# Performance work log

Hardware: AMD Instinct MI355X
Metric: run time of the kernel (lower is better)

Reference implementation:

```python
import jax, jax.numpy as jnp
import numpy as np

K = 30          # hard-coded in Hypergraph.from_feature_kNN(ft, k=30)
BN_EPS = 1e-5   # BatchNorm1d eval mode, running_mean=0, running_var=1


def setup_inputs() -> dict:
    key = jax.random.key(0)
    ks = jax.random.split(key, 3)
    B, C, H, W = 8, 64, 56, 56
    hid = 32
    return {
        "x": jax.random.normal(ks[0], (B, C, H, W), jnp.float32),
        "w1": jax.random.normal(ks[1], (C, hid), jnp.float32) / np.sqrt(C).astype(np.float32),
        "b1": jnp.zeros((hid,), jnp.float32),
        "g1": jnp.ones((hid,), jnp.float32),
        "be1": jnp.zeros((hid,), jnp.float32),
        "w2": jax.random.normal(ks[2], (hid, C), jnp.float32) / np.sqrt(hid).astype(np.float32),
        "b2": jnp.zeros((C,), jnp.float32),
        "g2": jnp.ones((C,), jnp.float32),
        "be2": jnp.zeros((C,), jnp.float32),
    }


def _knn_idx(ft, k):
    # squared euclidean distances via gram trick; same ordering as torch.cdist
    sq = jnp.sum(ft * ft, axis=1)
    d2 = sq[:, None] + sq[None, :] - 2.0 * (ft @ ft.T)   # [L, L]
    _, idx = jax.lax.top_k(-d2, k)                        # k smallest distances (incl. self)
    return idx                                            # [L, k] -> hyperedge e = kNN of vertex e


def _v2v_mean(X, nbr):
    # hg.v2v(X, aggr="mean"): v2e mean then e2v mean over the kNN incidence structure
    L, k = nbr.shape
    F = X.shape[1]
    Y = jnp.mean(X[nbr], axis=1)                                        # v2e: [L_edges, F]
    seg = nbr.reshape(-1)                                               # vertex nbr[e,j] belongs to edge e
    vals = jnp.broadcast_to(Y[:, None, :], (L, k, F)).reshape(L * k, F)
    s = jax.ops.segment_sum(vals, seg, num_segments=L)                  # e2v sum
    dv = jax.ops.segment_sum(jnp.ones((L * k,), X.dtype), seg, num_segments=L)
    return s / jnp.maximum(dv, 1.0)[:, None]                            # e2v mean


def _bn_eval(x, g, b):
    # BatchNorm1d in eval: running_mean=0, running_var=1
    return x * (g * np.float32(1.0 / np.sqrt(1.0 + BN_EPS))) + b


def reference(x, w1, b1, g1, be1, w2, b2, g2, be2):
    B, C, H, W = x.shape
    L = H * W
    xf = x.reshape(B, L, C)  # faithful raw x.view(B, L, C) (no transpose in source)

    def per_sample(ft):
        nbr = _knn_idx(ft, K)
        # HGNNPConv 1: theta -> bn -> v2v(mean) -> relu (dropout off in eval)
        h = _bn_eval(ft @ w1 + b1, g1, be1)
        h = jax.nn.relu(_v2v_mean(h, nbr))
        # HGNNPConv 2 (is_last): theta -> bn -> v2v(mean), no act/drop
        h = _bn_eval(h @ w2 + b2, g2, be2)
        return _v2v_mean(h, nbr)  # [L, C]

    outs = jax.vmap(per_sample)(xf)      # [B, L, C]
    return outs.reshape(B, -1, H, W)     # faithful raw outs.view(B, -1, H, W)
```

## Files before the change

kernel.cpp:

```cpp
#include <hip/hip_runtime.h>
#include <math.h>


namespace {

constexpr int cB = 8;
constexpr int cL = 3136;
constexpr int cC = 64;
constexpr int cH = 32;
constexpr int cK = 30;
constexpr int NV = cB * cL;
constexpr int QD = 10;
constexpr float BN_SC = 0.99999500003749964f;

typedef __bf16 bf16x4 __attribute__((ext_vector_type(4)));
typedef __bf16 bf16x8 __attribute__((ext_vector_type(8)));
typedef float floatx4 __attribute__((ext_vector_type(4)));

__device__ inline unsigned umin2(unsigned a, unsigned b) { return a < b ? a : b; }
__device__ inline unsigned umax2(unsigned a, unsigned b) { return a > b ? a : b; }
__device__ inline unsigned umin3(unsigned a, unsigned b, unsigned c) {
  return umin2(umin2(a, b), c);
}
__device__ inline float bf16lo(unsigned u) { return __uint_as_float(u << 16); }
__device__ inline float bf16hi(unsigned u) {
  return __uint_as_float(u & 0xFFFF0000u);
}

__device__ inline unsigned bclean64(unsigned v, int ln) {
#pragma unroll
  for (int off = 32; off; off >>= 1) {
    unsigned p = (unsigned)__shfl_xor((int)v, off);
    v = (ln & off) ? umax2(v, p) : umin2(v, p);
  }
  return v;
}

__global__ void k_split(const float* __restrict__ x, ushort* __restrict__ xhi,
                        ushort* __restrict__ xlo, float* __restrict__ sqf,
                        int* __restrict__ cnt, int* __restrict__ cur) {
  int v = blockIdx.x * 256 + threadIdx.x;
  if (v >= NV) return;
  cnt[v] = 0;
  cur[v] = 0;
  const float4* p = reinterpret_cast<const float4*>(x) + (size_t)v * 16;
  double s = 0.0;
#pragma unroll
  for (int c = 0; c < 16; ++c) {
    float4 f = p[c];
    bf16x4 hh, ll;
#pragma unroll
    for (int e = 0; e < 4; ++e) {
      float a = (&f.x)[e];
      __bf16 h = (__bf16)a;
      ll[e] = (__bf16)(a - (float)h);
      hh[e] = h;
      s += (double)a * (double)a;
    }
    *reinterpret_cast<bf16x4*>(&xhi[(size_t)v * 64 + c * 4]) = hh;
    *reinterpret_cast<bf16x4*>(&xlo[(size_t)v * 64 + c * 4]) = ll;
  }
  sqf[v] = (float)(s * 64.0 + 32768.0);
}

__global__ __launch_bounds__(128, 4) void k_sweep(
    const ushort* __restrict__ xhi, const ushort* __restrict__ xlo,
    const float* __restrict__ sqf, unsigned* __restrict__ candq) {
  const int ib = blockIdx.x, qt = blockIdx.y, b = blockIdx.z;
  const int r0 = ib * 32;
  const int jb0 = qt * 768;
  const int ntile = (qt == 3) ? 26 : 24;
  const size_t bbase = (size_t)b * cL;

  __shared__ ushort aHi[32 * 72], aLo[32 * 72];
  __shared__ ushort bHi[32 * 72], bLo[32 * 72];
  __shared__ float sqJs[32];

  const int t  = threadIdx.x;
  const int ln = t & 63;
  const int w  = t >> 6;
  const int tx = ln & 15;
  const int qd = ln >> 4;

#pragma unroll
  for (int it = 0; it < 2; ++it) {
    int idx = t + 128 * it;
    int r = idx >> 3, blk = idx & 7;
    *reinterpret_cast<uint4*>(&aHi[r * 72 + blk * 8]) =
        *reinterpret_cast<const uint4*>(&xhi[(bbase + r0 + r) * 64 + blk * 8]);
    *reinterpret_cast<uint4*>(&aLo[r * 72 + blk * 8]) =
        *reinterpret_cast<const uint4*>(&xlo[(bbase + r0 + r) * 64 + blk * 8]);
  }
  __syncthreads();

  bf16x8 aH[2], aL[2];
#pragma unroll
  for (int kk = 0; kk < 2; ++kk) {
    aH[kk] = *reinterpret_cast<const bf16x8*>(
        &aHi[(w * 16 + tx) * 72 + kk * 32 + qd * 8]);
    aL[kk] = *reinterpret_cast<const bf16x8*>(
        &aLo[(w * 16 + tx) * 72 + kk * 32 + qd * 8]);
  }

  unsigned q[4][QD];
#pragma unroll
  for (int e = 0; e < 4; ++e)
#pragma unroll
    for (int k = 0; k < QD; ++k) q[e][k] = 0xFFFFFFFFu;

  for (int st = 0; st < ntile; ++st) {
    const int jb = jb0 + st * 32;
#pragma unroll
    for (int it = 0; it < 2; ++it) {
      int idx = t + 128 * it;
      int r = idx >> 3, blk = idx & 7;
      *reinterpret_cast<uint4*>(&bHi[r * 72 + blk * 8]) =
          *reinterpret_cast<const uint4*>(&xhi[(bbase + jb + r) * 64 + blk * 8]);
      *reinterpret_cast<uint4*>(&bLo[r * 72 + blk * 8]) =
          *reinterpret_cast<const uint4*>(&xlo[(bbase + jb + r) * 64 + blk * 8]);
    }
    if (t < 32) sqJs[t] = sqf[bbase + jb + t];
    __syncthreads();

    unsigned pk[2][4];
#pragma unroll
    for (int f = 0; f < 2; ++f) {
      const int bro = (f * 16 + tx) * 72 + qd * 8;
      bf16x8 bh0 = *reinterpret_cast<const bf16x8*>(&bHi[bro]);
      bf16x8 bh1 = *reinterpret_cast<const bf16x8*>(&bHi[bro + 32]);
      bf16x8 bl0 = *reinterpret_cast<const bf16x8*>(&bLo[bro]);
      bf16x8 bl1 = *reinterpret_cast<const bf16x8*>(&bLo[bro + 32]);
      floatx4 acc = {0.f, 0.f, 0.f, 0.f};
      acc = __builtin_amdgcn_mfma_f32_16x16x32_bf16(aH[0], bh0, acc, 0, 0, 0);
      acc = __builtin_amdgcn_mfma_f32_16x16x32_bf16(aH[1], bh1, acc, 0, 0, 0);
      acc = __builtin_amdgcn_mfma_f32_16x16x32_bf16(aH[0], bl0, acc, 0, 0, 0);
      acc = __builtin_amdgcn_mfma_f32_16x16x32_bf16(aH[1], bl1, acc, 0, 0, 0);
      acc = __builtin_amdgcn_mfma_f32_16x16x32_bf16(aL[0], bh0, acc, 0, 0, 0);
      acc = __builtin_amdgcn_mfma_f32_16x16x32_bf16(aL[1], bh1, acc, 0, 0, 0);
      const float sjs = sqJs[f * 16 + tx];
      const unsigned col = (unsigned)(jb + f * 16 + tx);
#pragma unroll
      for (int e = 0; e < 4; ++e) {
        float qf = fmaf(acc[e], -128.f, sjs);
        qf = fminf(fmaxf(qf, 0.f), 65535.f);
        pk[f][e] = ((unsigned)qf << 12) | col;
      }
    }

#pragma unroll
    for (int e = 0; e < 4; ++e) {
      unsigned a0 = umin2(pk[0][e], pk[1][e]);
      unsigned a1 = umax2(pk[0][e], pk[1][e]);
#pragma unroll
      for (int i = QD - 1; i >= 2; --i)
        q[e][i] = umin3(q[e][i], umax2(q[e][i - 1], a0),
                        umax2(q[e][i - 2], a1));
      q[e][1] = umin3(q[e][1], umax2(q[e][0], a0), a1);
      q[e][0] = umin3(q[e][0], a0, a1);
    }
    __syncthreads();
  }

  unsigned* cr[4];
#pragma unroll
  for (int e = 0; e < 4; ++e)
    cr[e] = candq + (bbase + r0 + w * 16 + qd * 4 + e) * 160 + qt * 40;
  for (int it = 0; it < 40; ++it) {
    unsigned h0 = q[0][0], h1 = q[1][0], h2 = q[2][0], h3 = q[3][0];
    unsigned m0 = h0, m1 = h1, m2 = h2, m3 = h3;
#pragma unroll
    for (int off = 1; off < 16; off <<= 1) {
      m0 = umin2(m0, (unsigned)__shfl_xor((int)m0, off));
      m1 = umin2(m1, (unsigned)__shfl_xor((int)m1, off));
      m2 = umin2(m2, (unsigned)__shfl_xor((int)m2, off));
      m3 = umin2(m3, (unsigned)__shfl_xor((int)m3, off));
    }
    if (tx == 0) {
      cr[0][it] = m0;
      cr[1][it] = m1;
      cr[2][it] = m2;
      cr[3][it] = m3;
    }
    if (h0 == m0) {
#pragma unroll
      for (int k = 0; k < QD - 1; ++k) q[0][k] = q[0][k + 1];
      q[0][QD - 1] = 0xFFFFFFFFu;
    }
    if (h1 == m1) {
#pragma unroll
      for (int k = 0; k < QD - 1; ++k) q[1][k] = q[1][k + 1];
      q[1][QD - 1] = 0xFFFFFFFFu;
    }
    if (h2 == m2) {
#pragma unroll
      for (int k = 0; k < QD - 1; ++k) q[2][k] = q[2][k + 1];
      q[2][QD - 1] = 0xFFFFFFFFu;
    }
    if (h3 == m3) {
#pragma unroll
      for (int k = 0; k < QD - 1; ++k) q[3][k] = q[3][k + 1];
      q[3][QD - 1] = 0xFFFFFFFFu;
    }
  }
}

__global__ __launch_bounds__(256) void k_rescore(const float* __restrict__ x,
                                                 const unsigned* __restrict__ candq,
                                                 int* __restrict__ nbr,
                                                 int* __restrict__ cnt) {
  const int w  = threadIdx.x >> 6;
  const int ln = threadIdx.x & 63;
  const size_t row = (size_t)blockIdx.x * 4 + w;
  const size_t bvert = row - (row % cL);

  const unsigned* cq = candq + row * 160;
  unsigned A = (ln < 40) ? cq[ln]       : 0xFFFFFFFFu;
  unsigned B = (ln < 40) ? cq[40 + ln]  : 0xFFFFFFFFu;
  unsigned C = (ln < 40) ? cq[80 + ln]  : 0xFFFFFFFFu;
  unsigned D = (ln < 40) ? cq[120 + ln] : 0xFFFFFFFFu;

  unsigned s1 = umin2(A, (unsigned)__shfl((int)B, 63 - ln));
  s1 = bclean64(s1, ln);
  unsigned s2 = umin2(C, (unsigned)__shfl((int)D, 63 - ln));
  s2 = bclean64(s2, ln);
  unsigned g = umin2(s1, (unsigned)__shfl((int)s2, 63 - ln));
  g = bclean64(g, ln);

  const unsigned qv = g >> 12;
  const int col = min((int)(g & 0xFFFu), cL - 1);

  unsigned q29 = (unsigned)__shfl((int)qv, 29);
  unsigned q30 = (unsigned)__shfl((int)qv, 30);
  if (q30 > q29 + 3) {
    if (ln < cK) {
      nbr[row * cK + ln] = col;
      atomicAdd(&cnt[bvert + col], 1);
    }
    return;
  }

  float4 xi[16];
  const float4* xi4 = reinterpret_cast<const float4*>(x + row * 64);
#pragma unroll
  for (int c = 0; c < 16; ++c) xi[c] = xi4[c];

  double dv = 1e300;
  if (ln < 40) {
    const float4* xj4 = reinterpret_cast<const float4*>(x + (bvert + col) * 64);
    double ax = 0.0, ay = 0.0, az = 0.0, aw = 0.0;
#pragma unroll
    for (int c = 0; c < 16; ++c) {
      float4 xj = xj4[c];
      double d0 = (double)xi[c].x - (double)xj.x; ax = fma(d0, d0, ax);
      double d1 = (double)xi[c].y - (double)xj.y; ay = fma(d1, d1, ay);
      double d2 = (double)xi[c].z - (double)xj.z; az = fma(d2, d2, az);
      double d3 = (double)xi[c].w - (double)xj.w; aw = fma(d3, d3, aw);
    }
    dv = (ax + ay) + (az + aw);
  }
  int r2 = 0;
  for (int j = 0; j < 40; ++j) {
    double od = __shfl(dv, j);
    r2 += (od < dv || (od == dv && j < ln)) ? 1 : 0;
  }
  if (ln < 40 && r2 < cK) {
    nbr[row * cK + r2] = col;
    atomicAdd(&cnt[bvert + col], 1);
  }
}

__global__ void k_scan(const int* __restrict__ cnt, int* __restrict__ rp) {
  int b = blockIdx.x;
  int ln = threadIdx.x;
  const int* c = cnt + b * cL;
  int* r = rp + b * (cL + 1);
  int carry = 0;
  for (int base = 0; base < cL; base += 64) {
    int v = c[base + ln];
    int s = v;
#pragma unroll
    for (int off = 1; off < 64; off <<= 1) {
      int u = __shfl_up(s, off);
      if (ln >= off) s += u;
    }
    r[base + ln] = carry + s - v;
    carry += __shfl(s, 63);
  }
  if (ln == 63) r[cL] = carry;
}

__global__ void k_fill(const int* __restrict__ nbr, const int* __restrict__ rp,
                       int* __restrict__ cur, int* __restrict__ el) {
  int g = blockIdx.x * 256 + threadIdx.x;
  if (g >= NV * cK) return;
  int b = g / (cL * cK);
  int e = (g / cK) % cL;
  int v = nbr[g];
  v = min(max(v, 0), cL - 1);
  int p = rp[b * (cL + 1) + v] + atomicAdd(&cur[b * cL + v], 1);
  p = min(max(p, 0), cL * cK - 1);
  el[(size_t)b * cL * cK + p] = e;
}

__global__ __launch_bounds__(256) void k_theta1(const float* __restrict__ x,
                                                const float* __restrict__ w1,
                                                const float* __restrict__ b1,
                                                const float* __restrict__ g1,
                                                const float* __restrict__ be1,
                                                __bf16* __restrict__ h1) {
  __shared__ float w[cC * cH];
  int t = threadIdx.x;
  for (int n = t; n < cC * cH; n += 256) w[n] = w1[n];
  __syncthreads();
  int g = blockIdx.x * 256 + t;
  int row = g >> 5;
  int f = g & 31;
  const float4* xr = reinterpret_cast<const float4*>(x) + (size_t)row * 16;
  float s = 0.f;
#pragma unroll
  for (int kc = 0; kc < 16; ++kc) {
    float4 xv = xr[kc];
    s += xv.x * w[(4 * kc + 0) * cH + f];
    s += xv.y * w[(4 * kc + 1) * cH + f];
    s += xv.z * w[(4 * kc + 2) * cH + f];
    s += xv.w * w[(4 * kc + 3) * cH + f];
  }
  h1[g] = (__bf16)((s + b1[f]) * (g1[f] * BN_SC) + be1[f]);
}

__global__ __launch_bounds__(256) void k_v2e32(const __bf16* __restrict__ X,
                                               const int* __restrict__ nbr,
                                               __bf16* __restrict__ Y) {
  const int w  = threadIdx.x >> 6;
  const int ln = threadIdx.x & 63;
  const size_t er = (size_t)blockIdx.x * 4 + w;
  const size_t b  = er / cL;
  const __bf16* Xb = X + b * cL * cH;
  const int nb_l = nbr[er * cK + (ln < cK ? ln : cK - 1)];
  const int hi = ln >> 5, f = ln & 31;
  int idx[15];
#pragma unroll
  for (int m = 0; m < 15; ++m) idx[m] = __shfl(nb_l, hi + 2 * m);
  float y[15];
#pragma unroll
  for (int m = 0; m < 15; ++m) y[m] = (float)Xb[(size_t)idx[m] * cH + f];
  float s = 0.f;
#pragma unroll
  for (int m = 0; m < 15; ++m) s += y[m];
  s += __shfl_xor(s, 32);
  if (hi == 0) Y[er * cH + f] = (__bf16)(s * (1.f / 30.f));
}

__global__ __launch_bounds__(256) void k_e2v_t2(const __bf16* __restrict__ Y,
                                                const int* __restrict__ rp,
                                                const int* __restrict__ el,
                                                const float* __restrict__ w2,
                                                const float* __restrict__ b2,
                                                const float* __restrict__ g2,
                                                const float* __restrict__ be2,
                                                __bf16* __restrict__ h2) {
  __shared__ float w2s[cH * cC];
  {
    int t = threadIdx.x;
    for (int n = t; n < cH * cC; n += 256) w2s[n] = w2[n];
  }
  const int w  = threadIdx.x >> 6;
  const int ln = threadIdx.x & 63;
  const size_t vr = (size_t)blockIdx.x * 4 + w;
  const size_t b  = vr / cL;
  const int v = (int)(vr % cL);
  const int* rpb = rp + b * (cL + 1);
  const int s0 = rpb[v];
  const int deg = rpb[v + 1] - s0;
  const int* elb = el + b * (size_t)cL * cK + s0;
  const __bf16* Yb = Y + b * cL * cH;
  const int hi = ln >> 5, f = ln & 31;
  float s = 0.f;

  for (int base = 0; base < deg; base += 64) {
    const int take = min(64, deg - base);
    const int eidx = elb[base + (ln < take ? ln : 0)];
    for (int j0 = 0; j0 < take; j0 += 16) {
      float acc = 0.f;
#pragma unroll
      for (int k2 = 0; k2 < 8; ++k2) {
        int j = j0 + 2 * k2 + hi;
        int e0 = __shfl(eidx, j < take ? j : 0);
        float y = (float)Yb[(size_t)e0 * cH + f];
        acc += (j < take) ? y : 0.f;
      }
      s += acc;
    }
  }
  __syncthreads();

  s += __shfl_xor(s, 32);
  float r = fmaxf(s / (float)deg, 0.f);

  float s2 = 0.f;
#pragma unroll 8
  for (int k = 0; k < cH; ++k) {
    float rk = __shfl(r, k);
    s2 = fmaf(rk, w2s[k * cC + ln], s2);
  }
  h2[vr * cC + ln] = (__bf16)((s2 + b2[ln]) * (g2[ln] * BN_SC) + be2[ln]);
}

__global__ __launch_bounds__(256) void k_v2e64(const __bf16* __restrict__ X,
                                               const int* __restrict__ nbr,
                                               __bf16* __restrict__ Y) {
  const int w  = threadIdx.x >> 6;
  const int ln = threadIdx.x & 63;
  const size_t er = (size_t)blockIdx.x * 4 + w;
  const size_t b  = er / cL;
  const unsigned* Xb = reinterpret_cast<const unsigned*>(X + b * cL * cC);
  const int nb_l = nbr[er * cK + (ln < cK ? ln : cK - 1)];
  const int half = ln >> 5, f2 = ln & 31;
  int idx[15];
#pragma unroll
  for (int m = 0; m < 15; ++m) idx[m] = __shfl(nb_l, 2 * m + half);
  unsigned v[15];
#pragma unroll
  for (int m = 0; m < 15; ++m) v[m] = Xb[(size_t)idx[m] * 32 + f2];
  float s0 = 0.f, s1 = 0.f;
#pragma unroll
  for (int m = 0; m < 15; ++m) {
    s0 += bf16lo(v[m]);
    s1 += bf16hi(v[m]);
  }
  s0 += __shfl_xor(s0, 32);
  s1 += __shfl_xor(s1, 32);
  if (half == 0) {
    union {
      __bf16 h[2];
      unsigned u;
    } cv;
    cv.h[0] = (__bf16)(s0 * (1.f / 30.f));
    cv.h[1] = (__bf16)(s1 * (1.f / 30.f));
    reinterpret_cast<unsigned*>(Y)[er * 32 + f2] = cv.u;
  }
}

__global__ __launch_bounds__(256) void k_e2v64(const __bf16* __restrict__ Y,
                                               const int* __restrict__ rp,
                                               const int* __restrict__ el,
                                               float* __restrict__ out) {
  const int w  = threadIdx.x >> 6;
  const int ln = threadIdx.x & 63;
  const size_t vr = (size_t)blockIdx.x * 4 + w;
  const size_t b  = vr / cL;
  const int v = (int)(vr % cL);
  const int* rpb = rp + b * (cL + 1);
  const int s0r = rpb[v];
  const int deg = rpb[v + 1] - s0r;
  const int* elb = el + b * (size_t)cL * cK + s0r;
  const unsigned* Yb = reinterpret_cast<const unsigned*>(Y + b * cL * cC);
  const int half = ln >> 5, f2 = ln & 31;
  float s0 = 0.f, s1 = 0.f;

  for (int base = 0; base < deg; base += 64) {
    const int take = min(64, deg - base);
    const int eidx = elb[base + (ln < take ? ln : 0)];
    for (int j0 = 0; j0 < take; j0 += 16) {
      float a0 = 0.f, a1 = 0.f;
#pragma unroll
      for (int k2 = 0; k2 < 8; ++k2) {
        int j = j0 + 2 * k2 + half;
        int e0 = __shfl(eidx, j < take ? j : 0);
        unsigned u = Yb[(size_t)e0 * 32 + f2];
        bool ok = j < take;
        a0 += ok ? bf16lo(u) : 0.f;
        a1 += ok ? bf16hi(u) : 0.f;
      }
      s0 += a0;
      s1 += a1;
    }
  }
  s0 += __shfl_xor(s0, 32);
  s1 += __shfl_xor(s1, 32);
  float v0 = __shfl(s0, ln >> 1);
  float v1 = __shfl(s1, ln >> 1);
  out[vr * cC + ln] = ((ln & 1) ? v1 : v0) / (float)deg;
}

}

extern "C" void kernel_launch(void* const* d_in, const int* in_sizes, int n_in,
                              void* d_out, int out_size, void* d_ws,
                              size_t ws_size, hipStream_t stream) {
  (void)in_sizes; (void)n_in; (void)out_size; (void)ws_size;
  const float* x   = (const float*)d_in[0];
  const float* w1  = (const float*)d_in[1];
  const float* b1  = (const float*)d_in[2];
  const float* g1  = (const float*)d_in[3];
  const float* be1 = (const float*)d_in[4];
  const float* w2  = (const float*)d_in[5];
  const float* b2  = (const float*)d_in[6];
  const float* g2  = (const float*)d_in[7];
  const float* be2 = (const float*)d_in[8];
  float* out = (float*)d_out;

  char* base = (char*)d_ws;
  size_t off = 0;
  auto carve = [&](size_t bytes) {
    char* p = base + off;
    off += (bytes + 255) & ~(size_t)255;
    return p;
  };
  float* sqf = (float*)carve((size_t)NV * 4);
  int*   nbr = (int*)carve((size_t)NV * cK * 4);
  int*   rp  = (int*)carve((size_t)cB * (cL + 1) * 4);
  int*   cnt = (int*)carve((size_t)NV * 4);
  int*   cur = (int*)carve((size_t)NV * 4);
  char* RA = carve((size_t)NV * 64 * 2 * 2);
  ushort* xhi = (ushort*)RA;
  ushort* xlo = (ushort*)(RA + 3211264);
  int* el = (int*)RA;
  char* RC = carve((size_t)NV * 160 * 4);
  unsigned* candq = (unsigned*)RC;
  __bf16* h1 = (__bf16*)RC;
  __bf16* Y1 = (__bf16*)(RC + 1605632);
  __bf16* h2 = (__bf16*)(RC + 3211264);
  __bf16* Y2 = (__bf16*)(RC + 6422528);

  k_split<<<(NV + 255) / 256, 256, 0, stream>>>(x, xhi, xlo, sqf, cnt, cur);
  k_sweep<<<dim3(98, 4, cB), 128, 0, stream>>>(xhi, xlo, sqf, candq);
  k_rescore<<<NV / 4, 256, 0, stream>>>(x, candq, nbr, cnt);

  k_scan<<<cB, 64, 0, stream>>>(cnt, rp);
  k_fill<<<(NV * cK) / 256, 256, 0, stream>>>(nbr, rp, cur, el);

  k_theta1<<<NV * cH / 256, 256, 0, stream>>>(x, w1, b1, g1, be1, h1);
  k_v2e32<<<NV / 4, 256, 0, stream>>>(h1, nbr, Y1);
  k_e2v_t2<<<NV / 4, 256, 0, stream>>>(Y1, rp, el, w2, b2, g2, be2, h2);
  k_v2e64<<<NV / 4, 256, 0, stream>>>(h2, nbr, Y2);
  k_e2v64<<<NV / 4, 256, 0, stream>>>(Y2, rp, el, out);
}
```

Before: 425.1 us.

## Prefetch next B tile into registers in kNN sweep and parallelize scan

The kNN sweep kernel now loads the next 32-column tile of hi/lo bf16 features and squared norms into registers while the MFMA and top-k queue work runs on the current tile. The loads are written to shared memory at the top of the next iteration, so global latency overlaps with compute. A sched_barrier keeps the compiler from moving the prefetch. The per-batch prefix scan moves from one 64-thread wave looping serially over 3136 entries to a 1024-thread block doing a wave scan plus a cross-wave sum. In exchange the sweep uses more registers and the scan uses shared memory and a block barrier.

```diff
diff --git a/kernel.cpp b/kernel.cpp
--- a/kernel.cpp
+++ b/kernel.cpp
@@ -108,19 +108,37 @@
 #pragma unroll
     for (int k = 0; k < QD; ++k) q[e][k] = 0xFFFFFFFFu;
 
+  const int pr  = (t + 0)   >> 3, pblk  = (t + 0)   & 7;
+  const int pr1 = (t + 128) >> 3, pblk1 = (t + 128) & 7;
+  uint4 pH0, pH1, pL0, pL1;
+  float pS = 0.f;
+  {
+    const int jb = jb0;
+    pH0 = *reinterpret_cast<const uint4*>(&xhi[(bbase + jb + pr) * 64 + pblk * 8]);
+    pL0 = *reinterpret_cast<const uint4*>(&xlo[(bbase + jb + pr) * 64 + pblk * 8]);
+    pH1 = *reinterpret_cast<const uint4*>(&xhi[(bbase + jb + pr1) * 64 + pblk1 * 8]);
+    pL1 = *reinterpret_cast<const uint4*>(&xlo[(bbase + jb + pr1) * 64 + pblk1 * 8]);
+    if (t < 32) pS = sqf[bbase + jb + t];
+  }
+
   for (int st = 0; st < ntile; ++st) {
-    const int jb = jb0 + st * 32;
-#pragma unroll
-    for (int it = 0; it < 2; ++it) {
-      int idx = t + 128 * it;
-      int r = idx >> 3, blk = idx & 7;
-      *reinterpret_cast<uint4*>(&bHi[r * 72 + blk * 8]) =
-          *reinterpret_cast<const uint4*>(&xhi[(bbase + jb + r) * 64 + blk * 8]);
-      *reinterpret_cast<uint4*>(&bLo[r * 72 + blk * 8]) =
-          *reinterpret_cast<const uint4*>(&xlo[(bbase + jb + r) * 64 + blk * 8]);
-    }
-    if (t < 32) sqJs[t] = sqf[bbase + jb + t];
     __syncthreads();
+    *reinterpret_cast<uint4*>(&bHi[pr * 72 + pblk * 8])   = pH0;
+    *reinterpret_cast<uint4*>(&bLo[pr * 72 + pblk * 8])   = pL0;
+    *reinterpret_cast<uint4*>(&bHi[pr1 * 72 + pblk1 * 8]) = pH1;
+    *reinterpret_cast<uint4*>(&bLo[pr1 * 72 + pblk1 * 8]) = pL1;
+    if (t < 32) sqJs[t] = pS;
+    __syncthreads();
+
+    if (st + 1 < ntile) {
+      const int jb = jb0 + (st + 1) * 32;
+      pH0 = *reinterpret_cast<const uint4*>(&xhi[(bbase + jb + pr) * 64 + pblk * 8]);
+      pL0 = *reinterpret_cast<const uint4*>(&xlo[(bbase + jb + pr) * 64 + pblk * 8]);
+      pH1 = *reinterpret_cast<const uint4*>(&xhi[(bbase + jb + pr1) * 64 + pblk1 * 8]);
+      pL1 = *reinterpret_cast<const uint4*>(&xlo[(bbase + jb + pr1) * 64 + pblk1 * 8]);
+      if (t < 32) pS = sqf[bbase + jb + t];
+    }
+    __builtin_amdgcn_sched_barrier(0);
 
     unsigned pk[2][4];
 #pragma unroll
@@ -138,7 +156,7 @@
       acc = __builtin_amdgcn_mfma_f32_16x16x32_bf16(aL[0], bh0, acc, 0, 0, 0);
       acc = __builtin_amdgcn_mfma_f32_16x16x32_bf16(aL[1], bh1, acc, 0, 0, 0);
       const float sjs = sqJs[f * 16 + tx];
-      const unsigned col = (unsigned)(jb + f * 16 + tx);
+      const unsigned col = (unsigned)(jb0 + st * 32 + f * 16 + tx);
 #pragma unroll
       for (int e = 0; e < 4; ++e) {
         float qf = fmaf(acc[e], -128.f, sjs);
@@ -158,7 +176,6 @@
       q[e][1] = umin3(q[e][1], umax2(q[e][0], a0), a1);
       q[e][0] = umin3(q[e][0], a0, a1);
     }
-    __syncthreads();
   }
 
   unsigned* cr[4];
@@ -269,24 +286,43 @@
   }
 }
 
-__global__ void k_scan(const int* __restrict__ cnt, int* __restrict__ rp) {
-  int b = blockIdx.x;
-  int ln = threadIdx.x;
+__global__ __launch_bounds__(1024) void k_scan(const int* __restrict__ cnt,
+                                               int* __restrict__ rp) {
+  const int b = blockIdx.x;
   const int* c = cnt + b * cL;
   int* r = rp + b * (cL + 1);
+  const int t = threadIdx.x;
+  const int ln = t & 63, w = t >> 6;
+
+  int v[4];
+  int s = 0;
+#pragma unroll
+  for (int i = 0; i < 4; ++i) {
+    int idx = 4 * t + i;
+    v[i] = (idx < cL) ? c[idx] : 0;
+    s += v[i];
+  }
+  int inc = s;
+#pragma unroll
+  for (int off = 1; off < 64; off <<= 1) {
+    int u = __shfl_up(inc, off);
+    if (ln >= off) inc += u;
+  }
+  __shared__ int wsum[16];
+  if (ln == 63) wsum[w] = inc;
+  __syncthreads();
   int carry = 0;
-  for (int base = 0; base < cL; base += 64) {
-    int v = c[base + ln];
-    int s = v;
-#pragma unroll
-    for (int off = 1; off < 64; off <<= 1) {
-      int u = __shfl_up(s, off);
-      if (ln >= off) s += u;
-    }
-    r[base + ln] = carry + s - v;
-    carry += __shfl(s, 63);
-  }
-  if (ln == 63) r[cL] = carry;
+#pragma unroll
+  for (int i = 0; i < 16; ++i) carry += (i < w) ? wsum[i] : 0;
+
+  int excl = carry + inc - s;
+#pragma unroll
+  for (int i = 0; i < 4; ++i) {
+    int idx = 4 * t + i;
+    if (idx < cL) r[idx] = excl;
+    excl += v[i];
+  }
+  if (t == 1023) r[cL] = excl;
 }
 
 __global__ void k_fill(const int* __restrict__ nbr, const int* __restrict__ rp,
@@ -527,7 +563,7 @@
   k_sweep<<<dim3(98, 4, cB), 128, 0, stream>>>(xhi, xlo, sqf, candq);
   k_rescore<<<NV / 4, 256, 0, stream>>>(x, candq, nbr, cnt);
 
-  k_scan<<<cB, 64, 0, stream>>>(cnt, rp);
+  k_scan<<<cB, 1024, 0, stream>>>(cnt, rp);
   k_fill<<<(NV * cK) / 256, 256, 0, stream>>>(nbr, rp, cur, el);
 
   k_theta1<<<NV * cH / 256, 256, 0, stream>>>(x, w1, b1, g1, be1, h1);
```

Measured after the change: 402.9 us. 1.06x faster.
